# Performance work log

Hardware: AMD Instinct MI355X
Metric: run time of the kernel (lower is better)

Reference implementation:

```python
import jax, jax.numpy as jnp
import numpy as np


def setup_inputs() -> dict:
    key = jax.random.key(0)
    ks = jax.random.split(key, 8)
    N, NL, C, E, P3, P2, P1 = 2048, 16, 128, 10, 23, 4, 1
    return {
        "x": jax.random.normal(ks[0], (N, NL, C), dtype=jnp.float32),
        "atom_types": jax.random.randint(ks[1], (N,), 0, E),
        "U3": jax.random.normal(ks[2], (NL, NL, NL, P3), dtype=jnp.float32),
        "U2": jax.random.normal(ks[3], (NL, NL, P2), dtype=jnp.float32),
        "U1": jax.random.normal(ks[4], (NL, P1), dtype=jnp.float32),
        "W3": jax.random.normal(ks[5], (E, P3, C), dtype=jnp.float32),
        "W2": jax.random.normal(ks[6], (E, P2, C), dtype=jnp.float32),
        "W1": jax.random.normal(ks[7], (E, P1, C), dtype=jnp.float32),
    }


def reference(x, atom_types, U3, U2, U1, W3, W2, W1):
    # MACE symmetric contraction, correlation order 3, per-atom-type weights.
    # x: [N, nl, C]; atom_types: [N]; U3: [nl,nl,nl,P3]; W3: [E,P3,C]; etc.
    w3 = W3[atom_types]  # [N, P3, C]
    w2 = W2[atom_types]  # [N, P2, C]
    w1 = W1[atom_types]  # [N, P1, C]
    # Correlation-3 term: c3[n,a,b,c] = sum_{i,k} U3[a,b,i,k] * w3[n,k,c] * x[n,i,c]
    xw = jnp.einsum('nkc,nic->nkic', w3, x)        # [N, P3, nl, C]
    c3 = jnp.einsum('abik,nkic->nabc', U3, xw)     # [N, nl, nl, C]
    # Add correlation-2 term, contract one nl index with x.
    c2 = c3 + jnp.einsum('abk,nkc->nabc', U2, w2)  # [N, nl, nl, C]
    c1 = jnp.einsum('nabc,nbc->nac', c2, x)        # [N, nl, C]
    # Add correlation-1 term, contract last nl index with x.
    c1 = c1 + jnp.einsum('ak,nkc->nac', U1, w1)    # [N, nl, C]
    out = jnp.einsum('nac,nac->nc', c1, x)         # [N, C]
    return out
```

## Files before the change

### kernel.cpp

```cpp
#include <hip/hip_runtime.h>


constexpr int NL = 16;
constexpr int CC = 128;
constexpr int EE = 10;
constexpr int P3 = 23;
constexpr int P2 = 4;
constexpr int P1 = 1;
constexpr int NTRI = 816;
constexpr int NPAIR = 136;
constexpr int GG = 4;
constexpr int ASPLIT = 4;

constexpr int pairsBefore(int a) {
    int s = 0;
    for (int x = 0; x < a; x++) s += NL - x;
    return s;
}
constexpr int trisBefore(int a) {
    int s = 0;
    for (int x = 0; x < a; x++) s += (NL - x) * (NL - x + 1) / 2;
    return s;
}
static_assert(trisBefore(ASPLIT) % 4 == 0, "tri split must be float4-aligned");
static_assert(pairsBefore(ASPLIT) % 2 == 0, "pair split must be float2-aligned");

__global__ void k_symU(const float* __restrict__ U3, const float* __restrict__ U2,
                       float* __restrict__ U3s, float* __restrict__ U2s) {
    int idx = blockIdx.x * blockDim.x + threadIdx.x;
    if (idx < NTRI * P3) {
        int tri = idx / P3, k = idx % P3;
        int rem = tri, a = 0;
        while (rem >= (NL - a) * (NL - a + 1) / 2) { rem -= (NL - a) * (NL - a + 1) / 2; a++; }
        int b = a;
        while (rem >= NL - b) { rem -= NL - b; b++; }
        int i = b + rem;
        auto u = [&](int p, int q, int r) { return U3[((p * NL + q) * NL + r) * P3 + k]; };
        float s = u(a,b,i) + u(a,i,b) + u(b,a,i) + u(b,i,a) + u(i,a,b) + u(i,b,a);
        int m = (a == b && b == i) ? 6 : ((a == b || b == i) ? 2 : 1);
        U3s[idx] = s / (float)m;
    } else if (idx < NTRI * P3 + NPAIR * P2) {
        int j = idx - NTRI * P3;
        int pr = j / P2, k = j % P2;
        int rem = pr, a = 0;
        while (rem >= NL - a) { rem -= NL - a; a++; }
        int b = a + rem;
        float s = U2[(a * NL + b) * P2 + k];
        if (a != b) s += U2[(b * NL + a) * P2 + k];
        U2s[pr * P2 + k] = s;
    }
}

__global__ void k_buildA(const float* __restrict__ U3s, const float* __restrict__ U2s,
                         const float* __restrict__ U1,
                         const float* __restrict__ W3, const float* __restrict__ W2,
                         const float* __restrict__ W1,
                         float* __restrict__ A3, float* __restrict__ A2, float* __restrict__ A1) {
    int b = blockIdx.x;
    int c = threadIdx.x;
    if (b < EE * NTRI) {
        int t = b / NTRI, tri = b % NTRI;
        float s = 0.f;
        #pragma unroll
        for (int k = 0; k < P3; k++) s += U3s[tri * P3 + k] * W3[(t * P3 + k) * CC + c];
        A3[(((size_t)t * (NTRI / 4) + (tri >> 2)) * CC + c) * 4 + (tri & 3)] = s;
    } else if (b < EE * (NTRI + NPAIR)) {
        int j = b - EE * NTRI;
        int t = j / NPAIR, pr = j % NPAIR;
        float s = 0.f;
        #pragma unroll
        for (int k = 0; k < P2; k++) s += U2s[pr * P2 + k] * W2[(t * P2 + k) * CC + c];
        A2[(((size_t)t * (NPAIR / 2) + (pr >> 1)) * CC + c) * 2 + (pr & 1)] = s;
    } else {
        int t = b - EE * (NTRI + NPAIR);
        for (int a = 0; a < NL; a++) {
            float s = 0.f;
            #pragma unroll
            for (int k = 0; k < P1; k++) s += U1[a * P1 + k] * W1[(t * P1 + k) * CC + c];
            A1[((size_t)t * NL + a) * CC + c] = s;
        }
    }
}

__global__ void k_zero(int* counts) {
    if (threadIdx.x < 16) counts[threadIdx.x] = 0;
}

__global__ void k_bucket(const int* __restrict__ types, int* counts, int* buckets, int N) {
    int n = blockIdx.x * blockDim.x + threadIdx.x;
    if (n < N) {
        int t = types[n];
        int pos = atomicAdd(&counts[t], 1);
        buckets[t * N + pos] = n;
    }
}

__global__ void k_groups(const int* __restrict__ counts, const int* __restrict__ buckets,
                         int* __restrict__ groups, int* __restrict__ ngroups, int N) {
    __shared__ int goff[EE + 1];
    if (threadIdx.x == 0) {
        int off = 0;
        for (int t = 0; t < EE; t++) { goff[t] = off; off += (counts[t] + GG - 1) / GG; }
        goff[EE] = off;
        *ngroups = off;
    }
    __syncthreads();
    for (int t = 0; t < EE; t++) {
        int cnt = counts[t];
        int ng = (cnt + GG - 1) / GG;
        for (int g = threadIdx.x; g < ng; g += blockDim.x) {
            int* gr = &groups[(goff[t] + g) * 8];
            int nv = cnt - g * GG; if (nv > GG) nv = GG;
            gr[0] = t;
            gr[5] = nv;
            for (int j = 0; j < GG; j++) {
                int jj = j < nv ? j : nv - 1;
                gr[1 + j] = buckets[t * N + g * GG + jj];
            }
        }
    }
}

template <int A0, int A1, bool LIN>
__device__ __forceinline__ void eval_nest(const float (&xv)[GG][NL],
                                          const float4* __restrict__ a3v,
                                          const float2* __restrict__ a2v,
                                          const float* __restrict__ a1p,
                                          float (&acc)[GG]) {
    if (LIN) {
        #pragma unroll
        for (int a = 0; a < NL; a++) {
            float w = a1p[a * CC];
            #pragma unroll
            for (int g = 0; g < GG; g++) acc[g] += w * xv[g][a];
        }
    }
    float4 w4 = {0.f, 0.f, 0.f, 0.f};
    float2 wp = {0.f, 0.f};
    int tri = trisBefore(A0), pr = pairsBefore(A0);
    #pragma unroll
    for (int a = A0; a < A1; a++) {
        #pragma unroll
        for (int b = a; b < NL; b++) {
            float p[GG];
            #pragma unroll
            for (int g = 0; g < GG; g++) p[g] = xv[g][a] * xv[g][b];
            if ((pr & 1) == 0) wp = a2v[(size_t)(pr >> 1) * CC];
            float w2 = ((pr & 1) == 0) ? wp.x : wp.y;
            pr++;
            #pragma unroll
            for (int g = 0; g < GG; g++) acc[g] += w2 * p[g];
            #pragma unroll
            for (int i = b; i < NL; i++) {
                if ((tri & 3) == 0) w4 = a3v[(size_t)(tri >> 2) * CC];
                int r = tri & 3;
                float w3 = (r == 0) ? w4.x : (r == 1) ? w4.y : (r == 2) ? w4.z : w4.w;
                tri++;
                #pragma unroll
                for (int g = 0; g < GG; g++) acc[g] += w3 * (p[g] * xv[g][i]);
            }
        }
    }
}

__global__ __launch_bounds__(CC, 3) void k_main(const float* __restrict__ x,
                                                const float* __restrict__ A3,
                                                const float* __restrict__ A2,
                                                const float* __restrict__ A1,
                                                const int* __restrict__ groups,
                                                const int* __restrict__ ngroups,
                                                float* __restrict__ out) {
    int blk = blockIdx.x;
    if (blk >= *ngroups) return;
    const int* gr = groups + blk * 8;
    int t = gr[0];
    int nvalid = gr[5];
    int c = threadIdx.x;

    int na[GG];
    #pragma unroll
    for (int g = 0; g < GG; g++) na[g] = gr[1 + g];

    float xv[GG][NL];
    #pragma unroll
    for (int g = 0; g < GG; g++)
        #pragma unroll
        for (int i = 0; i < NL; i++)
            xv[g][i] = x[((size_t)na[g] * NL + i) * CC + c];

    const float4* a3v = (const float4*)A3 + (size_t)t * (NTRI / 4) * CC + c;
    const float2* a2v = (const float2*)A2 + (size_t)t * (NPAIR / 2) * CC + c;
    const float* a1p = A1 + (size_t)t * NL * CC + c;

    float acc[GG] = {0.f, 0.f, 0.f, 0.f};
    if (blockIdx.y == 0)
        eval_nest<0, ASPLIT, true>(xv, a3v, a2v, a1p, acc);
    else
        eval_nest<ASPLIT, NL, false>(xv, a3v, a2v, a1p, acc);

    #pragma unroll
    for (int g = 0; g < GG; g++)
        if (g < nvalid) atomicAdd(&out[(size_t)na[g] * CC + c], acc[g]);
}

extern "C" void kernel_launch(void* const* d_in, const int* in_sizes, int n_in,
                              void* d_out, int out_size, void* d_ws, size_t ws_size,
                              hipStream_t stream) {
    const float* x   = (const float*)d_in[0];
    const int* types = (const int*)d_in[1];
    const float* U3  = (const float*)d_in[2];
    const float* U2  = (const float*)d_in[3];
    const float* U1  = (const float*)d_in[4];
    const float* W3  = (const float*)d_in[5];
    const float* W2  = (const float*)d_in[6];
    const float* W1  = (const float*)d_in[7];
    float* out = (float*)d_out;
    int N = in_sizes[1];

    int ngmax = (N + GG - 1) / GG + EE;

    float* ws   = (float*)d_ws;
    float* U3s  = ws;
    float* U2s  = U3s + NTRI * P3;
    float* A3   = U2s + NPAIR * P2;
    float* A2   = A3 + (size_t)EE * NTRI * CC;
    float* A1   = A2 + (size_t)EE * NPAIR * CC;
    int* counts  = (int*)(A1 + (size_t)EE * NL * CC);
    int* buckets = counts + 16;
    int* groups  = buckets + (size_t)EE * N;
    int* ngroups = groups + (size_t)ngmax * 8;

    hipMemsetAsync(out, 0, (size_t)out_size * sizeof(float), stream);

    int symThreads = NTRI * P3 + NPAIR * P2;
    hipLaunchKernelGGL(k_symU, dim3((symThreads + 255) / 256), dim3(256), 0, stream,
                       U3, U2, U3s, U2s);
    hipLaunchKernelGGL(k_buildA, dim3(EE * (NTRI + NPAIR) + EE), dim3(CC), 0, stream,
                       U3s, U2s, U1, W3, W2, W1, A3, A2, A1);
    hipLaunchKernelGGL(k_zero, dim3(1), dim3(64), 0, stream, counts);
    hipLaunchKernelGGL(k_bucket, dim3((N + 255) / 256), dim3(256), 0, stream,
                       types, counts, buckets, N);
    hipLaunchKernelGGL(k_groups, dim3(1), dim3(256), 0, stream,
                       counts, buckets, groups, ngroups, N);
    hipLaunchKernelGGL(k_main, dim3(ngmax, 2), dim3(CC), 0, stream,
                       x, A3, A2, A1, groups, ngroups, out);
}
```

Baseline: 129.1 us.

## Factor symmetric contraction Horner-style, merge prep kernels, vectorize A-table build

The main kernel's triple loop is refactored Horner-style: the innermost sum over i is accumulated as a weighted sum of x, then multiplied by x[b] plus the pair weight, and finally by x[a] along with the linear term. This cuts the multiplies per triple and removes the per-pair product array. The bucketing, counting and grouping kernels are merged into one single-block kernel that counts in shared memory, removing two launches. k_buildA now computes four (or two) outputs per block with vector stores, so it launches fewer blocks. The main risk is that single-block bucketing serializes the prep step.

```diff
diff --git a/kernel.cpp b/kernel.cpp
--- a/kernel.cpp
+++ b/kernel.cpp
@@ -56,23 +56,36 @@
                          const float* __restrict__ W3, const float* __restrict__ W2,
                          const float* __restrict__ W1,
                          float* __restrict__ A3, float* __restrict__ A2, float* __restrict__ A1) {
+    constexpr int NB3 = EE * (NTRI / 4);
+    constexpr int NB2 = EE * (NPAIR / 2);
     int b = blockIdx.x;
     int c = threadIdx.x;
-    if (b < EE * NTRI) {
-        int t = b / NTRI, tri = b % NTRI;
-        float s = 0.f;
-        #pragma unroll
-        for (int k = 0; k < P3; k++) s += U3s[tri * P3 + k] * W3[(t * P3 + k) * CC + c];
-        A3[(((size_t)t * (NTRI / 4) + (tri >> 2)) * CC + c) * 4 + (tri & 3)] = s;
-    } else if (b < EE * (NTRI + NPAIR)) {
-        int j = b - EE * NTRI;
-        int t = j / NPAIR, pr = j % NPAIR;
-        float s = 0.f;
-        #pragma unroll
-        for (int k = 0; k < P2; k++) s += U2s[pr * P2 + k] * W2[(t * P2 + k) * CC + c];
-        A2[(((size_t)t * (NPAIR / 2) + (pr >> 1)) * CC + c) * 2 + (pr & 1)] = s;
+    if (b < NB3) {
+        int t = b / (NTRI / 4), tri4 = b % (NTRI / 4);
+        float4 sv = {0.f, 0.f, 0.f, 0.f};
+        #pragma unroll
+        for (int k = 0; k < P3; k++) {
+            float w = W3[(t * P3 + k) * CC + c];
+            sv.x += U3s[(tri4 * 4 + 0) * P3 + k] * w;
+            sv.y += U3s[(tri4 * 4 + 1) * P3 + k] * w;
+            sv.z += U3s[(tri4 * 4 + 2) * P3 + k] * w;
+            sv.w += U3s[(tri4 * 4 + 3) * P3 + k] * w;
+        }
+        ((float4*)A3)[((size_t)t * (NTRI / 4) + tri4) * CC + c] = sv;
+    } else if (b < NB3 + NB2) {
+        int j = b - NB3;
+        int t = j / (NPAIR / 2), pr2 = j % (NPAIR / 2);
+        float2 sv = {0.f, 0.f};
+        #pragma unroll
+        for (int k = 0; k < P2; k++) {
+            float w = W2[(t * P2 + k) * CC + c];
+            sv.x += U2s[(pr2 * 2 + 0) * P2 + k] * w;
+            sv.y += U2s[(pr2 * 2 + 1) * P2 + k] * w;
+        }
+        ((float2*)A2)[((size_t)t * (NPAIR / 2) + pr2) * CC + c] = sv;
     } else {
-        int t = b - EE * (NTRI + NPAIR);
+        int t = b - NB3 - NB2;
+        #pragma unroll
         for (int a = 0; a < NL; a++) {
             float s = 0.f;
             #pragma unroll
@@ -82,33 +95,30 @@
     }
 }
 
-__global__ void k_zero(int* counts) {
-    if (threadIdx.x < 16) counts[threadIdx.x] = 0;
-}
-
-__global__ void k_bucket(const int* __restrict__ types, int* counts, int* buckets, int N) {
-    int n = blockIdx.x * blockDim.x + threadIdx.x;
-    if (n < N) {
+__global__ void k_prep(const int* __restrict__ types, int* __restrict__ buckets,
+                       int* __restrict__ groups, int* __restrict__ ngroups, int N) {
+    __shared__ int scnt[EE];
+    __shared__ int goff[EE + 1];
+    int tid = threadIdx.x;
+    if (tid < EE) scnt[tid] = 0;
+    __syncthreads();
+    for (int n = tid; n < N; n += blockDim.x) {
         int t = types[n];
-        int pos = atomicAdd(&counts[t], 1);
+        int pos = atomicAdd(&scnt[t], 1);
         buckets[t * N + pos] = n;
     }
-}
-
-__global__ void k_groups(const int* __restrict__ counts, const int* __restrict__ buckets,
-                         int* __restrict__ groups, int* __restrict__ ngroups, int N) {
-    __shared__ int goff[EE + 1];
-    if (threadIdx.x == 0) {
+    __syncthreads();
+    if (tid == 0) {
         int off = 0;
-        for (int t = 0; t < EE; t++) { goff[t] = off; off += (counts[t] + GG - 1) / GG; }
+        for (int t = 0; t < EE; t++) { goff[t] = off; off += (scnt[t] + GG - 1) / GG; }
         goff[EE] = off;
         *ngroups = off;
     }
     __syncthreads();
     for (int t = 0; t < EE; t++) {
-        int cnt = counts[t];
+        int cnt = scnt[t];
         int ng = (cnt + GG - 1) / GG;
-        for (int g = threadIdx.x; g < ng; g += blockDim.x) {
+        for (int g = tid; g < ng; g += blockDim.x) {
             int* gr = &groups[(goff[t] + g) * 8];
             int nv = cnt - g * GG; if (nv > GG) nv = GG;
             gr[0] = t;
@@ -121,45 +131,49 @@
     }
 }
 
-template <int A0, int A1, bool LIN>
+template <int A0, int A1e>
 __device__ __forceinline__ void eval_nest(const float (&xv)[GG][NL],
                                           const float4* __restrict__ a3v,
                                           const float2* __restrict__ a2v,
                                           const float* __restrict__ a1p,
                                           float (&acc)[GG]) {
-    if (LIN) {
-        #pragma unroll
-        for (int a = 0; a < NL; a++) {
-            float w = a1p[a * CC];
-            #pragma unroll
-            for (int g = 0; g < GG; g++) acc[g] += w * xv[g][a];
-        }
-    }
     float4 w4 = {0.f, 0.f, 0.f, 0.f};
     float2 wp = {0.f, 0.f};
     int tri = trisBefore(A0), pr = pairsBefore(A0);
     #pragma unroll
-    for (int a = A0; a < A1; a++) {
+    for (int a = A0; a < A1e; a++) {
+        float w1 = a1p[a * CC];
+        float q[GG];
+        #pragma unroll
+        for (int g = 0; g < GG; g++) q[g] = w1;
         #pragma unroll
         for (int b = a; b < NL; b++) {
-            float p[GG];
-            #pragma unroll
-            for (int g = 0; g < GG; g++) p[g] = xv[g][a] * xv[g][b];
-            if ((pr & 1) == 0) wp = a2v[(size_t)(pr >> 1) * CC];
-            float w2 = ((pr & 1) == 0) ? wp.x : wp.y;
-            pr++;
-            #pragma unroll
-            for (int g = 0; g < GG; g++) acc[g] += w2 * p[g];
-            #pragma unroll
-            for (int i = b; i < NL; i++) {
-                if ((tri & 3) == 0) w4 = a3v[(size_t)(tri >> 2) * CC];
+            if ((tri & 3) == 0) w4 = a3v[(size_t)(tri >> 2) * CC];
+            {
                 int r = tri & 3;
                 float w3 = (r == 0) ? w4.x : (r == 1) ? w4.y : (r == 2) ? w4.z : w4.w;
                 tri++;
+                float s[GG];
                 #pragma unroll
-                for (int g = 0; g < GG; g++) acc[g] += w3 * (p[g] * xv[g][i]);
+                for (int g = 0; g < GG; g++) s[g] = w3 * xv[g][b];
+                #pragma unroll
+                for (int i = b + 1; i < NL; i++) {
+                    if ((tri & 3) == 0) w4 = a3v[(size_t)(tri >> 2) * CC];
+                    int ri = tri & 3;
+                    float w3i = (ri == 0) ? w4.x : (ri == 1) ? w4.y : (ri == 2) ? w4.z : w4.w;
+                    tri++;
+                    #pragma unroll
+                    for (int g = 0; g < GG; g++) s[g] += w3i * xv[g][i];
+                }
+                if ((pr & 1) == 0) wp = a2v[(size_t)(pr >> 1) * CC];
+                float w2 = ((pr & 1) == 0) ? wp.x : wp.y;
+                pr++;
+                #pragma unroll
+                for (int g = 0; g < GG; g++) q[g] += xv[g][b] * (w2 + s[g]);
             }
         }
+        #pragma unroll
+        for (int g = 0; g < GG; g++) acc[g] += xv[g][a] * q[g];
     }
 }
 
@@ -194,9 +208,9 @@
 
     float acc[GG] = {0.f, 0.f, 0.f, 0.f};
     if (blockIdx.y == 0)
-        eval_nest<0, ASPLIT, true>(xv, a3v, a2v, a1p, acc);
+        eval_nest<0, ASPLIT>(xv, a3v, a2v, a1p, acc);
     else
-        eval_nest<ASPLIT, NL, false>(xv, a3v, a2v, a1p, acc);
+        eval_nest<ASPLIT, NL>(xv, a3v, a2v, a1p, acc);
 
     #pragma unroll
     for (int g = 0; g < GG; g++)
@@ -225,8 +239,7 @@
     float* A3   = U2s + NPAIR * P2;
     float* A2   = A3 + (size_t)EE * NTRI * CC;
     float* A1   = A2 + (size_t)EE * NPAIR * CC;
-    int* counts  = (int*)(A1 + (size_t)EE * NL * CC);
-    int* buckets = counts + 16;
+    int* buckets = (int*)(A1 + (size_t)EE * NL * CC);
     int* groups  = buckets + (size_t)EE * N;
     int* ngroups = groups + (size_t)ngmax * 8;
 
@@ -235,13 +248,10 @@
     int symThreads = NTRI * P3 + NPAIR * P2;
     hipLaunchKernelGGL(k_symU, dim3((symThreads + 255) / 256), dim3(256), 0, stream,
                        U3, U2, U3s, U2s);
-    hipLaunchKernelGGL(k_buildA, dim3(EE * (NTRI + NPAIR) + EE), dim3(CC), 0, stream,
-                       U3s, U2s, U1, W3, W2, W1, A3, A2, A1);
-    hipLaunchKernelGGL(k_zero, dim3(1), dim3(64), 0, stream, counts);
-    hipLaunchKernelGGL(k_bucket, dim3((N + 255) / 256), dim3(256), 0, stream,
-                       types, counts, buckets, N);
-    hipLaunchKernelGGL(k_groups, dim3(1), dim3(256), 0, stream,
-                       counts, buckets, groups, ngroups, N);
+    hipLaunchKernelGGL(k_buildA, dim3(EE * (NTRI / 4) + EE * (NPAIR / 2) + EE), dim3(CC), 0,
+                       stream, U3s, U2s, U1, W3, W2, W1, A3, A2, A1);
+    hipLaunchKernelGGL(k_prep, dim3(1), dim3(256), 0, stream,
+                       types, buckets, groups, ngroups, N);
     hipLaunchKernelGGL(k_main, dim3(ngmax, 2), dim3(CC), 0, stream,
                        x, A3, A2, A1, groups, ngroups, out);
 }
```

Measured after the change: 318.2 us. +146.6%, slower.
